# Kernel tuning notes

Measured on AMD Instinct MI355X. Metric: run time of the kernel, lower is better.

Reference implementation:

```python
import jax, jax.numpy as jnp
import numpy as np

DELTA = 1e-3  # inverse-distance kernel smoothing from NEC paper
NUM_NEIGHBOURS = 50


def setup_inputs() -> dict:
    key = jax.random.key(0)
    k1, k2, k3 = jax.random.split(key, 3)
    B, C, D = 1024, 500000, 64
    return {
        "keys": jax.random.normal(k1, (B, D), dtype=jnp.float32),
        "table_keys": jax.random.normal(k2, (C, D), dtype=jnp.float32),
        "table_values": jax.random.normal(k3, (C,), dtype=jnp.float32),
    }


def reference(keys, table_keys, table_values):
    # Brute-force kNN search: squared L2 distances [B, C]
    d2 = (
        jnp.sum(keys * keys, axis=1, keepdims=True)
        - 2.0 * (keys @ table_keys.T)
        + jnp.sum(table_keys * table_keys, axis=1)[None, :]
    )
    _, idx = jax.lax.top_k(-d2, NUM_NEIGHBOURS)  # [B, K] smallest distances

    neighbours = table_keys[idx]  # [B, K, D] gather
    # recompute exact squared distances against gathered neighbours
    sq = jnp.sum((keys[:, None, :] - neighbours) ** 2, axis=2)  # [B, K]
    w = 1.0 / (sq + DELTA)
    w = w / jnp.sum(w, axis=1, keepdims=True)
    v = table_values[idx]  # [B, K]
    return jnp.sum(w * v, axis=1)  # [B]
```

## Files before the change

### kernel.cpp

```cpp
#include <hip/hip_runtime.h>
#include <math.h>


#define DELTA_SMOOTH 1e-3f
#define K_NEIGH 50
#define MAXCAP 8192
#define NBINS 256
#define MARGIN_T 1.5f
#define MARGIN_Q 26
#define RPB 1024
#define QTILE 512
#define SDEPTH 6
#define LW 768
#define CVL 2048
#define S_SAMP 16384
#define T_SAMP 13
#define FSAMPLE 2048
#define FTARGET 6
#define FMARGIN 0.75f
#define FQB 4

typedef __attribute__((ext_vector_type(8))) short short8;
typedef __attribute__((ext_vector_type(4))) float f32x4;
typedef __attribute__((address_space(1))) const unsigned int g_u32;
typedef __attribute__((address_space(3))) unsigned int l_u32;

__device__ __forceinline__ unsigned f2bf(float f) {
  unsigned u = __float_as_uint(f);
  return ((u + 0x7fffu + ((u >> 16) & 1u)) >> 16) & 0xffffu;
}

__global__ __launch_bounds__(256) void convert_kernel(
    const float* __restrict__ tk, uint4* __restrict__ tkbf,
    float* __restrict__ tnh2, int C, int padded) {
  int t = blockIdx.x * 256 + threadIdx.x;
  int r = t >> 3;
  if (r >= padded) return;
  int c = t & 7;
  int rs = r < C ? r : C - 1;
  const float4* src = (const float4*)(tk + (size_t)rs * 64 + c * 8);
  float4 a = src[0], b = src[1];
  float sq = a.x * a.x + a.y * a.y + a.z * a.z + a.w * a.w
           + b.x * b.x + b.y * b.y + b.z * b.z + b.w * b.w;
  sq += __shfl_xor(sq, 1); sq += __shfl_xor(sq, 2); sq += __shfl_xor(sq, 4);
  if (c == 0) tnh2[r] = (r < C) ? sq * 0.5f : 3e38f;
  uint4 u;
  u.x = f2bf(a.x) | (f2bf(a.y) << 16);
  u.y = f2bf(a.z) | (f2bf(a.w) << 16);
  u.z = f2bf(b.x) | (f2bf(b.y) << 16);
  u.w = f2bf(b.z) | (f2bf(b.w) << 16);
  tkbf[(size_t)(r >> 6) * 512 + (r & 63) * 8 + (c ^ (r & 7))] = u;
}

__global__ __launch_bounds__(512, 4) void qthresh_mfma(
    const uint4* __restrict__ tkbf, const float* __restrict__ keys,
    const float* __restrict__ tnh2, unsigned short* __restrict__ dsamp) {
  __shared__ __align__(16) uint4 bstage[2][512];
  __shared__ float tnh_lds[128];
  int tid = threadIdx.x;
  int qt = blockIdx.x & 1;
  int chunk = blockIdx.x >> 1;
  int qbase = qt * QTILE;
  int rstart = chunk * 128;
  if (tid < 128) tnh_lds[tid] = tnh2[rstart + tid];
  int lane = tid & 63, wq = tid >> 6, l15 = lane & 15, quad = lane >> 4;
  short8 afrag[4][2];
  #pragma unroll
  for (int mt = 0; mt < 4; ++mt) {
    const float* kp = keys + (size_t)(qbase + wq * 64 + mt * 16 + l15) * 64 + quad * 8;
    #pragma unroll
    for (int s = 0; s < 2; ++s) {
      float4 x = *(const float4*)(kp + s * 32);
      float4 y = *(const float4*)(kp + s * 32 + 4);
      short8 a;
      a[0] = (short)f2bf(x.x); a[1] = (short)f2bf(x.y);
      a[2] = (short)f2bf(x.z); a[3] = (short)f2bf(x.w);
      a[4] = (short)f2bf(y.x); a[5] = (short)f2bf(y.y);
      a[6] = (short)f2bf(y.z); a[7] = (short)f2bf(y.w);
      afrag[mt][s] = a;
    }
  }
  const uint4* gbase = tkbf + (size_t)(rstart >> 6) * 512;
  __builtin_amdgcn_global_load_lds((g_u32*)(gbase + tid),
                                   (l_u32*)(&bstage[0][wq * 64]), 16, 0, 0);
  __syncthreads();
  f32x4 zero4 = {0.f, 0.f, 0.f, 0.f};
  for (int it = 0; it < 2; ++it) {
    if (it == 0)
      __builtin_amdgcn_global_load_lds((g_u32*)(gbase + 512 + tid),
                                       (l_u32*)(&bstage[1][wq * 64]), 16, 0, 0);
    const unsigned char* buf = (const unsigned char*)bstage[it & 1];
    #pragma unroll
    for (int half = 0; half < 2; ++half) {
      short8 b[2][2];
      #pragma unroll
      for (int tt = 0; tt < 2; ++tt) {
        int nloc = half * 32 + tt * 16 + l15;
        #pragma unroll
        for (int s = 0; s < 2; ++s) {
          int c = s * 4 + quad;
          unsigned addr = (unsigned)(nloc * 128 + ((c ^ (nloc & 7)) << 4));
          b[tt][s] = *(const short8*)(buf + addr);
        }
      }
      f32x4 acc[4][2];
      #pragma unroll
      for (int mt = 0; mt < 4; ++mt)
        #pragma unroll
        for (int tt = 0; tt < 2; ++tt) {
          f32x4 a0 = __builtin_amdgcn_mfma_f32_16x16x32_bf16(afrag[mt][0], b[tt][0], zero4, 0, 0, 0);
          acc[mt][tt] = __builtin_amdgcn_mfma_f32_16x16x32_bf16(afrag[mt][1], b[tt][1], a0, 0, 0, 0);
        }
      #pragma unroll
      for (int tt = 0; tt < 2; ++tt) {
        int rloc = it * 64 + half * 32 + tt * 16 + l15;
        float tnh = tnh_lds[rloc];
        int n = rstart + rloc;
        #pragma unroll
        for (int mt = 0; mt < 4; ++mt) {
          #pragma unroll
          for (int r = 0; r < 4; ++r) {
            int ql = wq * 64 + mt * 16 + quad * 4 + r;
            int u = (int)fmaf(tnh - acc[mt][tt][r], 512.f, 32768.f);
            u = u < 0 ? 0 : (u > 65535 ? 65535 : u);
            dsamp[(size_t)(qbase + ql) * S_SAMP + n] = (unsigned short)u;
          }
        }
      }
    }
    __syncthreads();
  }
}

__global__ __launch_bounds__(256) void qthresh_scan(
    const unsigned short* __restrict__ dsamp, float* __restrict__ thrh,
    int* __restrict__ cnt) {
  int q = blockIdx.x;
  __shared__ unsigned hist[512];
  int tid = threadIdx.x;
  hist[tid] = 0u; hist[tid + 256] = 0u;
  __syncthreads();
  const unsigned short* dp = dsamp + (size_t)q * S_SAMP;
  for (int i = tid; i < S_SAMP; i += 256) atomicAdd(&hist[dp[i] >> 7], 1u);
  __syncthreads();
  if (tid == 0) {
    unsigned cum = 0; int bstar = 511;
    for (int b = 0; b < 512; ++b) {
      cum += hist[b];
      if (cum >= (unsigned)T_SAMP) { bstar = b; break; }
    }
    float thr = (float)(bstar + 1) * 0.5f - 128.f + MARGIN_T;
    thrh[q] = 0.5f * thr;
    cnt[q] = 0;
  }
}

__global__ __launch_bounds__(512, 4) void filter_mfma_fast(
    const uint4* __restrict__ tkbf, const float* __restrict__ keys,
    const float* __restrict__ tnh2, const float* __restrict__ thrh,
    int* __restrict__ cnt, unsigned* __restrict__ candi, int C, int cap) {
  __shared__ __align__(16) uint4 bstage[4][512];
  __shared__ float tnh_lds[RPB];
  __shared__ float thr_lds[QTILE];
  __shared__ unsigned scnt[QTILE];
  __shared__ unsigned sbuf[QTILE * SDEPTH];

  int tid = threadIdx.x;
  int qt = blockIdx.x & 1;
  int chunk = blockIdx.x >> 1;
  int qbase = qt * QTILE;
  int rstart = chunk * RPB;

  tnh_lds[tid] = tnh2[rstart + tid];
  tnh_lds[tid + 512] = tnh2[rstart + tid + 512];
  thr_lds[tid] = thrh[qbase + tid];
  scnt[tid] = 0u;

  int lane = tid & 63, wq = tid >> 6, l15 = lane & 15, quad = lane >> 4;

  short8 afrag[4][2];
  #pragma unroll
  for (int mt = 0; mt < 4; ++mt) {
    const float* kp = keys + (size_t)(qbase + wq * 64 + mt * 16 + l15) * 64 + quad * 8;
    #pragma unroll
    for (int s = 0; s < 2; ++s) {
      float4 x = *(const float4*)(kp + s * 32);
      float4 y = *(const float4*)(kp + s * 32 + 4);
      short8 a;
      a[0] = (short)f2bf(x.x); a[1] = (short)f2bf(x.y);
      a[2] = (short)f2bf(x.z); a[3] = (short)f2bf(x.w);
      a[4] = (short)f2bf(y.x); a[5] = (short)f2bf(y.y);
      a[6] = (short)f2bf(y.z); a[7] = (short)f2bf(y.w);
      afrag[mt][s] = a;
    }
  }

  __syncthreads();

  float thrr[4][4];
  #pragma unroll
  for (int mt = 0; mt < 4; ++mt)
    #pragma unroll
    for (int r = 0; r < 4; ++r)
      thrr[mt][r] = thr_lds[wq * 64 + mt * 16 + quad * 4 + r];

  const uint4* gbase = tkbf + (size_t)(rstart >> 6) * 512;
  const int PHASES = RPB / 128;
  #pragma unroll
  for (int s = 0; s < 2; ++s)
    __builtin_amdgcn_global_load_lds((g_u32*)(gbase + (size_t)s * 512 + tid),
                                     (l_u32*)(&bstage[s][wq * 64]), 16, 0, 0);

  f32x4 zero4 = {0.f, 0.f, 0.f, 0.f};

  for (int ph = 0; ph < PHASES; ++ph) {
    __builtin_amdgcn_s_barrier();
    if (ph + 1 < PHASES) {
      #pragma unroll
      for (int s = 0; s < 2; ++s)
        __builtin_amdgcn_global_load_lds(
            (g_u32*)(gbase + ((size_t)(ph + 1) * 2 + s) * 512 + tid),
            (l_u32*)(&bstage[(((ph + 1) * 2 + s)) & 3][wq * 64]), 16, 0, 0);
      asm volatile("s_waitcnt vmcnt(2)" ::: "memory");
    } else {
      asm volatile("s_waitcnt vmcnt(0)" ::: "memory");
    }
    __builtin_amdgcn_sched_barrier(0);
    #pragma unroll
    for (int sl = 0; sl < 2; ++sl) {
      const unsigned char* buf = (const unsigned char*)bstage[(ph * 2 + sl) & 3];
      int itrow = ph * 128 + sl * 64;
      #pragma unroll
      for (int half = 0; half < 2; ++half) {
        short8 b[2][2];
        #pragma unroll
        for (int tt = 0; tt < 2; ++tt) {
          int nloc = half * 32 + tt * 16 + l15;
          #pragma unroll
          for (int s = 0; s < 2; ++s) {
            int c = s * 4 + quad;
            unsigned addr = (unsigned)(nloc * 128 + ((c ^ (nloc & 7)) << 4));
            b[tt][s] = *(const short8*)(buf + addr);
          }
        }
        f32x4 acc[4][2];
        #pragma unroll
        for (int mt = 0; mt < 4; ++mt)
          #pragma unroll
          for (int tt = 0; tt < 2; ++tt) {
            f32x4 a0 = __builtin_amdgcn_mfma_f32_16x16x32_bf16(afrag[mt][0], b[tt][0], zero4, 0, 0, 0);
            acc[mt][tt] = __builtin_amdgcn_mfma_f32_16x16x32_bf16(afrag[mt][1], b[tt][1], a0, 0, 0, 0);
          }
        #pragma unroll
        for (int tt = 0; tt < 2; ++tt) {
          int rloc = itrow + half * 32 + tt * 16 + l15;
          float tnh = tnh_lds[rloc];
          int n = rstart + rloc;
          #pragma unroll
          for (int mt = 0; mt < 4; ++mt) {
            #pragma unroll
            for (int r = 0; r < 4; ++r) {
              float t = tnh - acc[mt][tt][r];
              if (__builtin_expect(t < thrr[mt][r], 0)) {
                int ql = wq * 64 + mt * 16 + quad * 4 + r;
                int d2q = (int)fmaf(t, 32.f, 2048.f);
                d2q = d2q < 0 ? 0 : (d2q > 8191 ? 8191 : d2q);
                unsigned v = ((unsigned)d2q << 19) | (unsigned)n;
                unsigned p = atomicAdd(&scnt[ql], 1u);
                if (p < SDEPTH) {
                  sbuf[ql * SDEPTH + p] = v;
                } else {
                  int g = atomicAdd(&cnt[qbase + ql], 1);
                  if (g < cap) candi[(size_t)(qbase + ql) * cap + g] = v;
                }
              }
            }
          }
        }
      }
    }
  }
  __syncthreads();
  int m = (int)scnt[tid];
  if (m > SDEPTH) m = SDEPTH;
  if (m > 0) {
    int base = atomicAdd(&cnt[qbase + tid], m);
    for (int j = 0; j < m; ++j) {
      int g = base + j;
      if (g < cap) candi[(size_t)(qbase + tid) * cap + g] = sbuf[tid * SDEPTH + j];
    }
  }
}

__global__ __launch_bounds__(256) void qthresh_fb(
    const float* __restrict__ keys, const float* __restrict__ tk,
    float* __restrict__ thr, float* __restrict__ qnorm, int C) {
  int q0 = blockIdx.x * FQB;
  __shared__ __align__(16) float kq[FQB * 64];
  __shared__ unsigned hist[FQB][NBINS];
  __shared__ float qn4[FQB];
  int tid = threadIdx.x;
  for (int i = tid; i < FQB * 64; i += 256) kq[i] = keys[(size_t)q0 * 64 + i];
  for (int i = tid; i < FQB * NBINS; i += 256) (&hist[0][0])[i] = 0u;
  __syncthreads();
  if (tid < FQB) {
    float s = 0.f;
    for (int j = 0; j < 64; ++j) { float v = kq[tid * 64 + j]; s += v * v; }
    qn4[tid] = s;
  }
  __syncthreads();
  int kc = tid & 3;
  const float4* kq4 = (const float4*)kq;
  float4 kf[FQB][4];
  #pragma unroll
  for (int jq = 0; jq < FQB; ++jq)
    #pragma unroll
    for (int u = 0; u < 4; ++u) kf[jq][u] = kq4[jq * 16 + kc * 4 + u];
  int S = FSAMPLE < C ? FSAMPLE : C;
  for (int r = tid >> 2; r < S; r += 64) {
    const float4* trow = (const float4*)(tk + (size_t)r * 64 + kc * 16);
    float4 t0 = trow[0], t1 = trow[1], t2 = trow[2], t3 = trow[3];
    float tn = t0.x * t0.x + t0.y * t0.y + t0.z * t0.z + t0.w * t0.w
             + t1.x * t1.x + t1.y * t1.y + t1.z * t1.z + t1.w * t1.w
             + t2.x * t2.x + t2.y * t2.y + t2.z * t2.z + t2.w * t2.w
             + t3.x * t3.x + t3.y * t3.y + t3.z * t3.z + t3.w * t3.w;
    tn += __shfl_xor(tn, 1); tn += __shfl_xor(tn, 2);
    float dot[FQB];
    #pragma unroll
    for (int jq = 0; jq < FQB; ++jq) {
      float s = kf[jq][0].x * t0.x + kf[jq][0].y * t0.y + kf[jq][0].z * t0.z + kf[jq][0].w * t0.w
              + kf[jq][1].x * t1.x + kf[jq][1].y * t1.y + kf[jq][1].z * t1.z + kf[jq][1].w * t1.w
              + kf[jq][2].x * t2.x + kf[jq][2].y * t2.y + kf[jq][2].z * t2.z + kf[jq][2].w * t2.w
              + kf[jq][3].x * t3.x + kf[jq][3].y * t3.y + kf[jq][3].z * t3.z + kf[jq][3].w * t3.w;
      s += __shfl_xor(s, 1); s += __shfl_xor(s, 2);
      dot[jq] = s;
    }
    if (kc == 0) {
      #pragma unroll
      for (int jq = 0; jq < FQB; ++jq) {
        float d2 = qn4[jq] + tn - 2.f * dot[jq];
        int b = (int)d2;
        b = b < 0 ? 0 : (b > NBINS - 1 ? NBINS - 1 : b);
        atomicAdd(&hist[jq][b], 1u);
      }
    }
  }
  __syncthreads();
  if (tid < FQB) {
    unsigned cum = 0; int bstar = NBINS - 1;
    for (int b = 0; b < NBINS; ++b) {
      cum += hist[tid][b];
      if (cum >= (unsigned)FTARGET) { bstar = b; break; }
    }
    thr[q0 + tid] = (float)(bstar + 1) + FMARGIN - qn4[tid];
    qnorm[q0 + tid] = qn4[tid];
  }
}

__global__ __launch_bounds__(512, 4) void filter_fb(
    const float* __restrict__ keys, const float* __restrict__ tk,
    const float* __restrict__ thr, const float* __restrict__ qnorm,
    int* __restrict__ cnt, unsigned* __restrict__ candi, int C, int cap) {
  __shared__ float tnstage[64];
  __shared__ float thr_lds[QTILE];
  __shared__ float qn_lds[QTILE];
  __shared__ unsigned scnt[QTILE];
  __shared__ unsigned sbuf[QTILE * SDEPTH];
  __shared__ __align__(16) unsigned char bstage[64 * 128];
  int tid = threadIdx.x;
  int qt = blockIdx.x & 1;
  int chunk = blockIdx.x >> 1;
  int qbase = qt * QTILE;
  int rstart = chunk * RPB;
  thr_lds[tid] = thr[qbase + tid];
  qn_lds[tid] = qnorm[qbase + tid];
  scnt[tid] = 0u;
  int lane = tid & 63, wq = tid >> 6, l15 = lane & 15, quad = lane >> 4;
  short8 afrag[4][2];
  #pragma unroll
  for (int mt = 0; mt < 4; ++mt) {
    const float* kp = keys + (size_t)(qbase + wq * 64 + mt * 16 + l15) * 64 + quad * 8;
    #pragma unroll
    for (int s = 0; s < 2; ++s) {
      float4 x = *(const float4*)(kp + s * 32);
      float4 y = *(const float4*)(kp + s * 32 + 4);
      short8 a;
      a[0] = (short)f2bf(x.x); a[1] = (short)f2bf(x.y);
      a[2] = (short)f2bf(x.z); a[3] = (short)f2bf(x.w);
      a[4] = (short)f2bf(y.x); a[5] = (short)f2bf(y.y);
      a[6] = (short)f2bf(y.z); a[7] = (short)f2bf(y.w);
      afrag[mt][s] = a;
    }
  }
  __syncthreads();
  float hq[4];
  #pragma unroll
  for (int mt = 0; mt < 4; ++mt) {
    float h0 = thr_lds[wq * 64 + mt * 16 + quad * 4 + 0];
    float h1 = thr_lds[wq * 64 + mt * 16 + quad * 4 + 1];
    float h2 = thr_lds[wq * 64 + mt * 16 + quad * 4 + 2];
    float h3 = thr_lds[wq * 64 + mt * 16 + quad * 4 + 3];
    hq[mt] = fmaxf(fmaxf(h0, h1), fmaxf(h2, h3));
  }
  int srow = tid >> 3, scol = tid & 7;
  unsigned sbyte = (unsigned)(srow * 128 + ((scol ^ (srow & 7)) << 4));
  const int ITERS = RPB / 64;
  int r0 = rstart + srow; if (r0 > C - 1) r0 = C - 1;
  float4 pa = *(const float4*)(tk + (size_t)r0 * 64 + scol * 8);
  float4 pb = *(const float4*)(tk + (size_t)r0 * 64 + scol * 8 + 4);
  f32x4 zero4 = {0.f, 0.f, 0.f, 0.f};
  for (int it = 0; it < ITERS; ++it) {
    float part = pa.x * pa.x + pa.y * pa.y + pa.z * pa.z + pa.w * pa.w
               + pb.x * pb.x + pb.y * pb.y + pb.z * pb.z + pb.w * pb.w;
    part += __shfl_xor(part, 1); part += __shfl_xor(part, 2); part += __shfl_xor(part, 4);
    if ((tid & 7) == 0) tnstage[srow] = part;
    uint4 u;
    u.x = f2bf(pa.x) | (f2bf(pa.y) << 16);
    u.y = f2bf(pa.z) | (f2bf(pa.w) << 16);
    u.z = f2bf(pb.x) | (f2bf(pb.y) << 16);
    u.w = f2bf(pb.z) | (f2bf(pb.w) << 16);
    *(uint4*)(bstage + sbyte) = u;
    __syncthreads();
    if (it + 1 < ITERS) {
      int rn = rstart + (it + 1) * 64 + srow; if (rn > C - 1) rn = C - 1;
      pa = *(const float4*)(tk + (size_t)rn * 64 + scol * 8);
      pb = *(const float4*)(tk + (size_t)rn * 64 + scol * 8 + 4);
    }
    #pragma unroll
    for (int half = 0; half < 2; ++half) {
      short8 b[2][2];
      #pragma unroll
      for (int tt = 0; tt < 2; ++tt) {
        int nloc = half * 32 + tt * 16 + l15;
        #pragma unroll
        for (int s = 0; s < 2; ++s) {
          int c = s * 4 + quad;
          unsigned addr = (unsigned)(nloc * 128 + ((c ^ (nloc & 7)) << 4));
          b[tt][s] = *(const short8*)(bstage + addr);
        }
      }
      f32x4 acc[4][2];
      #pragma unroll
      for (int mt = 0; mt < 4; ++mt)
        #pragma unroll
        for (int tt = 0; tt < 2; ++tt) {
          f32x4 a0 = __builtin_amdgcn_mfma_f32_16x16x32_bf16(afrag[mt][0], b[tt][0], zero4, 0, 0, 0);
          acc[mt][tt] = __builtin_amdgcn_mfma_f32_16x16x32_bf16(afrag[mt][1], b[tt][1], a0, 0, 0, 0);
        }
      #pragma unroll
      for (int tt = 0; tt < 2; ++tt) {
        float tn = tnstage[half * 32 + tt * 16 + l15];
        int n = rstart + it * 64 + half * 32 + tt * 16 + l15;
        #pragma unroll
        for (int mt = 0; mt < 4; ++mt) {
          float d0 = fmaf(-2.f, acc[mt][tt][0], tn);
          float d1 = fmaf(-2.f, acc[mt][tt][1], tn);
          float d2 = fmaf(-2.f, acc[mt][tt][2], tn);
          float d3 = fmaf(-2.f, acc[mt][tt][3], tn);
          float mn4 = fminf(fminf(d0, d1), fminf(d2, d3));
          if (mn4 < hq[mt]) {
            float dd[4] = {d0, d1, d2, d3};
            #pragma unroll
            for (int r = 0; r < 4; ++r) {
              int ql = wq * 64 + mt * 16 + quad * 4 + r;
              if (dd[r] < thr_lds[ql] && n < C) {
                float d2f = dd[r] + qn_lds[ql];
                int d2q = (int)(d2f * 16.f);
                d2q = d2q < 0 ? 0 : (d2q > 8191 ? 8191 : d2q);
                unsigned v = ((unsigned)d2q << 19) | (unsigned)n;
                unsigned p = atomicAdd(&scnt[ql], 1u);
                if (p < SDEPTH) sbuf[ql * SDEPTH + p] = v;
                else {
                  int g = atomicAdd(&cnt[qbase + ql], 1);
                  if (g < cap) candi[(size_t)(qbase + ql) * cap + g] = v;
                }
              }
            }
          }
        }
      }
    }
    __syncthreads();
  }
  int m = (int)scnt[tid];
  if (m > SDEPTH) m = SDEPTH;
  if (m > 0) {
    int base = atomicAdd(&cnt[qbase + tid], m);
    for (int j = 0; j < m; ++j) {
      int g = base + j;
      if (g < cap) candi[(size_t)(qbase + tid) * cap + g] = sbuf[tid * SDEPTH + j];
    }
  }
}

__global__ __launch_bounds__(256) void select_kernel(
    const float* __restrict__ keys, const float* __restrict__ tk,
    const float* __restrict__ tv, const int* __restrict__ cnt,
    const unsigned* __restrict__ candi, float* __restrict__ out, int cap) {
  int q = blockIdx.x;
  __shared__ unsigned cvl[CVL];
  __shared__ unsigned hist[NBINS];
  __shared__ unsigned wsum[4];
  __shared__ unsigned minq_sh;
  __shared__ int b50_sh;
  __shared__ int lidx[LW];
  __shared__ unsigned ed2[LW];
  __shared__ int m_sh;
  __shared__ float redw[4], redwv[4];
  int tid = threadIdx.x;
  int lane = tid & 63;
  int wid = tid >> 6;
  int n = cnt[q];
  if (n > cap) n = cap;
  hist[tid] = 0u;
  if (tid == 0) { minq_sh = 0xffffffffu; b50_sh = NBINS - 1; m_sh = 0; }
  __syncthreads();
  const unsigned* cv = candi + (size_t)q * cap;
  unsigned mn = 0xffffffffu;
  for (int i = tid; i < n; i += 256) {
    unsigned v = cv[i];
    if (i < CVL) cvl[i] = v;
    unsigned d = v >> 19; if (d < mn) mn = d;
  }
  #pragma unroll
  for (int off = 1; off < 64; off <<= 1) { unsigned o = __shfl_xor(mn, off); if (o < mn) mn = o; }
  if (lane == 0) atomicMin(&minq_sh, mn);
  __syncthreads();
  unsigned base = minq_sh;
  for (int i = tid; i < n; i += 256) {
    unsigned v = (i < CVL) ? cvl[i] : cv[i];
    unsigned d = (v >> 19) - base;
    unsigned b = d >> 1; if (b > NBINS - 1) b = NBINS - 1;
    atomicAdd(&hist[b], 1u);
  }
  __syncthreads();
  unsigned h = hist[tid];
  unsigned p = h;
  #pragma unroll
  for (int off = 1; off < 64; off <<= 1) {
    unsigned v = __shfl_up(p, off);
    if (lane >= off) p += v;
  }
  if (lane == 63) wsum[wid] = p;
  __syncthreads();
  unsigned add = 0;
  for (int w2 = 0; w2 < wid; ++w2) add += wsum[w2];
  p += add;
  if (p >= (unsigned)K_NEIGH && p - h < (unsigned)K_NEIGH) b50_sh = tid;
  __syncthreads();
  unsigned Tq = base + (((unsigned)(b50_sh + 1)) << 1) + MARGIN_Q;
  for (int i = tid; i < n; i += 256) {
    unsigned v = (i < CVL) ? cvl[i] : cv[i];
    if ((v >> 19) <= Tq) {
      int p2 = atomicAdd(&m_sh, 1);
      if (p2 < LW) lidx[p2] = (int)(v & 0x7ffffu);
    }
  }
  __syncthreads();
  int m = m_sh; if (m > LW) m = LW;
  float kqv = keys[(size_t)q * 64 + lane];
  for (int i0 = wid * 4; i0 < m; i0 += 16) {
    int mm = m - i0; if (mm > 4) mm = 4;
    int idx[4]; float t[4];
    for (int u = 0; u < mm; ++u) idx[u] = lidx[i0 + u];
    for (int u = 0; u < mm; ++u) t[u] = tk[(size_t)idx[u] * 64 + lane];
    for (int u = 0; u < mm; ++u) {
      float d = t[u] - kqv;
      float s = d * d;
      #pragma unroll
      for (int off = 1; off < 64; off <<= 1) s += __shfl_xor(s, off);
      if (lane == 0) ed2[i0 + u] = __float_as_uint(s);
    }
  }
  __syncthreads();
  float accw = 0.f, accwv = 0.f;
  for (int i = tid; i < m; i += 256) {
    unsigned long long key = ((unsigned long long)ed2[i] << 19) | (unsigned)lidx[i];
    int rank = 0;
    for (int j = 0; j < m; ++j) {
      unsigned long long kj = ((unsigned long long)ed2[j] << 19) | (unsigned)lidx[j];
      rank += (kj < key) ? 1 : 0;
    }
    if (rank < K_NEIGH) {
      float d2 = __uint_as_float(ed2[i]);
      float w = 1.f / (d2 + DELTA_SMOOTH);
      accw += w;
      accwv += w * tv[lidx[i]];
    }
  }
  #pragma unroll
  for (int off = 1; off < 64; off <<= 1) {
    accw += __shfl_xor(accw, off);
    accwv += __shfl_xor(accwv, off);
  }
  if (lane == 0) { redw[wid] = accw; redwv[wid] = accwv; }
  __syncthreads();
  if (tid == 0) {
    float sw = redw[0] + redw[1] + redw[2] + redw[3];
    float swv = redwv[0] + redwv[1] + redwv[2] + redwv[3];
    out[q] = swv / sw;
  }
}

extern "C" void kernel_launch(void* const* d_in, const int* in_sizes, int n_in,
                              void* d_out, int out_size, void* d_ws, size_t ws_size,
                              hipStream_t stream) {
  const float* keys = (const float*)d_in[0];
  const float* tk   = (const float*)d_in[1];
  const float* tv   = (const float*)d_in[2];
  float* out = (float*)d_out;
  int B = in_sizes[0] / 64;
  int C = in_sizes[2];

  int nchunks = (C + RPB - 1) / RPB;
  int padded = nchunks * RPB;

  char* w = (char*)d_ws;
  float* thrh = (float*)w;  w += (size_t)B * 4;
  float* qnfb = (float*)w;  w += (size_t)B * 4;
  int*   cnt  = (int*)w;    w += (size_t)B * 4;
  size_t fixed = (size_t)(w - (char*)d_ws);

  size_t tk_bytes = (size_t)padded * 128 + (size_t)padded * 4;
  size_t dsamp_bytes = (size_t)S_SAMP * (size_t)B * 2;
  size_t region = ws_size > fixed + tk_bytes ? ws_size - fixed - tk_bytes : 0;
  bool fast = region >= dsamp_bytes && region >= 2048ull * (size_t)B * 4;

  if (fast) {
    uint4* tkbf = (uint4*)w;              w += (size_t)padded * 128;
    float* tnh2 = (float*)w;              w += (size_t)padded * 4;
    unsigned short* dsamp = (unsigned short*)w;
    unsigned* candi = (unsigned*)w;
    int cap = (int)(region / (4ull * (size_t)B));
    if (cap > MAXCAP) cap = MAXCAP;
    convert_kernel<<<(padded * 8 + 255) / 256, 256, 0, stream>>>(tk, tkbf, tnh2, C, padded);
    qthresh_mfma<<<256, 512, 0, stream>>>(tkbf, keys, tnh2, dsamp);
    qthresh_scan<<<B, 256, 0, stream>>>(dsamp, thrh, cnt);
    filter_mfma_fast<<<nchunks * 2, 512, 0, stream>>>(tkbf, keys, tnh2, thrh,
                                                      cnt, candi, C, cap);
    select_kernel<<<B, 256, 0, stream>>>(keys, tk, tv, cnt, candi, out, cap);
  } else {
    unsigned* candi = (unsigned*)w;
    int cap = (int)((ws_size - fixed) / (4ull * (size_t)B));
    if (cap > MAXCAP) cap = MAXCAP;
    if (cap < 1) cap = 1;
    hipMemsetAsync(cnt, 0, (size_t)B * 4, stream);
    qthresh_fb<<<B / FQB, 256, 0, stream>>>(keys, tk, thrh, qnfb, C);
    filter_fb<<<nchunks * 2, 512, 0, stream>>>(keys, tk, thrh, qnfb,
                                               cnt, candi, C, cap);
    select_kernel<<<B, 256, 0, stream>>>(keys, tk, tv, cnt, candi, out, cap);
  }
}
```

Baseline: 379.0 us.

## Cover all 1024 queries per filter block to halve table-tile loads

The filter kernel now runs 1024-thread blocks that each handle all 1024 queries against one 1024-row table chunk, instead of two 512-query blocks per chunk. Each bf16 table tile is loaded into LDS once rather than twice, cutting global traffic and the block count. The staging pipeline moves from per-128-row prefetch with partial waitcnt to double-buffered pairs with a full vmcnt(0)+barrier, and the per-query LDS spill depth drops from 6 to 4. The cost is higher LDS per block, lower occupancy, less load/compute overlap, and more global atomic overflow.

New measurement: 953.5 us. 2.52x slower.

```diff
diff --git a/kernel.cpp b/kernel.cpp
--- a/kernel.cpp
+++ b/kernel.cpp
@@ -9,6 +9,8 @@
 #define MARGIN_T 1.5f
 #define MARGIN_Q 26
 #define RPB 1024
+#define QB 1024
+#define SDF 4
 #define QTILE 512
 #define SDEPTH 6
 #define LW 768
@@ -60,7 +62,7 @@
   int tid = threadIdx.x;
   int qt = blockIdx.x & 1;
   int chunk = blockIdx.x >> 1;
-  int qbase = qt * QTILE;
+  int qbase = qt * 512;
   int rstart = chunk * 128;
   if (tid < 128) tnh_lds[tid] = tnh2[rstart + tid];
   int lane = tid & 63, wq = tid >> 6, l15 = lane & 15, quad = lane >> 4;
@@ -155,25 +157,21 @@
   }
 }
 
-__global__ __launch_bounds__(512, 4) void filter_mfma_fast(
+__global__ __launch_bounds__(1024, 8) void filter_mfma_fast(
     const uint4* __restrict__ tkbf, const float* __restrict__ keys,
     const float* __restrict__ tnh2, const float* __restrict__ thrh,
     int* __restrict__ cnt, unsigned* __restrict__ candi, int C, int cap) {
   __shared__ __align__(16) uint4 bstage[4][512];
   __shared__ float tnh_lds[RPB];
-  __shared__ float thr_lds[QTILE];
-  __shared__ unsigned scnt[QTILE];
-  __shared__ unsigned sbuf[QTILE * SDEPTH];
+  __shared__ float thr_lds[QB];
+  __shared__ unsigned scnt[QB];
+  __shared__ unsigned sbuf[QB * SDF];
 
   int tid = threadIdx.x;
-  int qt = blockIdx.x & 1;
-  int chunk = blockIdx.x >> 1;
-  int qbase = qt * QTILE;
-  int rstart = chunk * RPB;
+  int rstart = blockIdx.x * RPB;
 
   tnh_lds[tid] = tnh2[rstart + tid];
-  tnh_lds[tid + 512] = tnh2[rstart + tid + 512];
-  thr_lds[tid] = thrh[qbase + tid];
+  thr_lds[tid] = thrh[tid];
   scnt[tid] = 0u;
 
   int lane = tid & 63, wq = tid >> 6, l15 = lane & 15, quad = lane >> 4;
@@ -181,7 +179,7 @@
   short8 afrag[4][2];
   #pragma unroll
   for (int mt = 0; mt < 4; ++mt) {
-    const float* kp = keys + (size_t)(qbase + wq * 64 + mt * 16 + l15) * 64 + quad * 8;
+    const float* kp = keys + (size_t)(wq * 64 + mt * 16 + l15) * 64 + quad * 8;
     #pragma unroll
     for (int s = 0; s < 2; ++s) {
       float4 x = *(const float4*)(kp + s * 32);
@@ -205,31 +203,24 @@
       thrr[mt][r] = thr_lds[wq * 64 + mt * 16 + quad * 4 + r];
 
   const uint4* gbase = tkbf + (size_t)(rstart >> 6) * 512;
-  const int PHASES = RPB / 128;
-  #pragma unroll
-  for (int s = 0; s < 2; ++s)
-    __builtin_amdgcn_global_load_lds((g_u32*)(gbase + (size_t)s * 512 + tid),
-                                     (l_u32*)(&bstage[s][wq * 64]), 16, 0, 0);
+  const int PAIRS = RPB / 128;
+  __builtin_amdgcn_global_load_lds((g_u32*)(gbase + tid),
+                                   (l_u32*)((uint4*)&bstage[0][0] + wq * 64), 16, 0, 0);
 
   f32x4 zero4 = {0.f, 0.f, 0.f, 0.f};
 
-  for (int ph = 0; ph < PHASES; ++ph) {
-    __builtin_amdgcn_s_barrier();
-    if (ph + 1 < PHASES) {
-      #pragma unroll
-      for (int s = 0; s < 2; ++s)
-        __builtin_amdgcn_global_load_lds(
-            (g_u32*)(gbase + ((size_t)(ph + 1) * 2 + s) * 512 + tid),
-            (l_u32*)(&bstage[(((ph + 1) * 2 + s)) & 3][wq * 64]), 16, 0, 0);
-      asm volatile("s_waitcnt vmcnt(2)" ::: "memory");
-    } else {
-      asm volatile("s_waitcnt vmcnt(0)" ::: "memory");
-    }
+  for (int p = 0; p < PAIRS; ++p) {
+    asm volatile("s_waitcnt vmcnt(0)\n\ts_barrier" ::: "memory");
     __builtin_amdgcn_sched_barrier(0);
+    if (p + 1 < PAIRS) {
+      __builtin_amdgcn_global_load_lds(
+          (g_u32*)(gbase + (size_t)(p + 1) * 1024 + tid),
+          (l_u32*)((uint4*)&bstage[((p + 1) & 1) * 2][0] + wq * 64), 16, 0, 0);
+    }
     #pragma unroll
     for (int sl = 0; sl < 2; ++sl) {
-      const unsigned char* buf = (const unsigned char*)bstage[(ph * 2 + sl) & 3];
-      int itrow = ph * 128 + sl * 64;
+      const unsigned char* buf = (const unsigned char*)&bstage[(p & 1) * 2 + sl][0];
+      int itrow = p * 128 + sl * 64;
       #pragma unroll
       for (int half = 0; half < 2; ++half) {
         short8 b[2][2];
@@ -266,12 +257,12 @@
                 int d2q = (int)fmaf(t, 32.f, 2048.f);
                 d2q = d2q < 0 ? 0 : (d2q > 8191 ? 8191 : d2q);
                 unsigned v = ((unsigned)d2q << 19) | (unsigned)n;
-                unsigned p = atomicAdd(&scnt[ql], 1u);
-                if (p < SDEPTH) {
-                  sbuf[ql * SDEPTH + p] = v;
+                unsigned pp = atomicAdd(&scnt[ql], 1u);
+                if (pp < SDF) {
+                  sbuf[ql * SDF + pp] = v;
                 } else {
-                  int g = atomicAdd(&cnt[qbase + ql], 1);
-                  if (g < cap) candi[(size_t)(qbase + ql) * cap + g] = v;
+                  int g = atomicAdd(&cnt[ql], 1);
+                  if (g < cap) candi[(size_t)ql * cap + g] = v;
                 }
               }
             }
@@ -282,12 +273,12 @@
   }
   __syncthreads();
   int m = (int)scnt[tid];
-  if (m > SDEPTH) m = SDEPTH;
+  if (m > SDF) m = SDF;
   if (m > 0) {
-    int base = atomicAdd(&cnt[qbase + tid], m);
+    int base = atomicAdd(&cnt[tid], m);
     for (int j = 0; j < m; ++j) {
       int g = base + j;
-      if (g < cap) candi[(size_t)(qbase + tid) * cap + g] = sbuf[tid * SDEPTH + j];
+      if (g < cap) candi[(size_t)tid * cap + g] = sbuf[tid * SDF + j];
     }
   }
 }
@@ -636,8 +627,8 @@
     convert_kernel<<<(padded * 8 + 255) / 256, 256, 0, stream>>>(tk, tkbf, tnh2, C, padded);
     qthresh_mfma<<<256, 512, 0, stream>>>(tkbf, keys, tnh2, dsamp);
     qthresh_scan<<<B, 256, 0, stream>>>(dsamp, thrh, cnt);
-    filter_mfma_fast<<<nchunks * 2, 512, 0, stream>>>(tkbf, keys, tnh2, thrh,
-                                                      cnt, candi, C, cap);
+    filter_mfma_fast<<<nchunks, 1024, 0, stream>>>(tkbf, keys, tnh2, thrh,
+                                                   cnt, candi, C, cap);
     select_kernel<<<B, 256, 0, stream>>>(keys, tk, tv, cnt, candi, out, cap);
   } else {
     unsigned* candi = (unsigned*)w;
```

## Halve threshold sample, fold norm into MFMA accumulator, simplify filter pipeline

Applied to the files above, without the earlier changes.

Cuts the threshold-estimation sample from 16384 to 8192 rows (with a lower target rank) so the qthresh kernels do half the work. The filter kernel now seeds the MFMA accumulator with the negated half-norm, which removes a subtraction per output element, and compares against a negated threshold. Its prefetch loop changes to a wait-all-then-barrier pattern. The smaller sample may give a looser threshold and more candidates. Full waits could also expose load latency that the old partial wait hid.

After: 388.5 us. +2.5%, slower.

```diff
diff --git a/kernel.cpp b/kernel.cpp
--- a/kernel.cpp
+++ b/kernel.cpp
@@ -13,8 +13,8 @@
 #define SDEPTH 6
 #define LW 768
 #define CVL 2048
-#define S_SAMP 16384
-#define T_SAMP 13
+#define S_SAMP 8192
+#define T_SAMP 8
 #define FSAMPLE 2048
 #define FTARGET 6
 #define FMARGIN 0.75f
@@ -60,7 +60,7 @@
   int tid = threadIdx.x;
   int qt = blockIdx.x & 1;
   int chunk = blockIdx.x >> 1;
-  int qbase = qt * QTILE;
+  int qbase = qt * 512;
   int rstart = chunk * 128;
   if (tid < 128) tnh_lds[tid] = tnh2[rstart + tid];
   int lane = tid & 63, wq = tid >> 6, l15 = lane & 15, quad = lane >> 4;
@@ -197,41 +197,42 @@
 
   __syncthreads();
 
-  float thrr[4][4];
+  float negthr[4][4];
   #pragma unroll
   for (int mt = 0; mt < 4; ++mt)
     #pragma unroll
     for (int r = 0; r < 4; ++r)
-      thrr[mt][r] = thr_lds[wq * 64 + mt * 16 + quad * 4 + r];
+      negthr[mt][r] = -thr_lds[wq * 64 + mt * 16 + quad * 4 + r];
 
   const uint4* gbase = tkbf + (size_t)(rstart >> 6) * 512;
-  const int PHASES = RPB / 128;
+  const int PAIRS = RPB / 128;
   #pragma unroll
   for (int s = 0; s < 2; ++s)
     __builtin_amdgcn_global_load_lds((g_u32*)(gbase + (size_t)s * 512 + tid),
-                                     (l_u32*)(&bstage[s][wq * 64]), 16, 0, 0);
-
-  f32x4 zero4 = {0.f, 0.f, 0.f, 0.f};
-
-  for (int ph = 0; ph < PHASES; ++ph) {
-    __builtin_amdgcn_s_barrier();
-    if (ph + 1 < PHASES) {
-      #pragma unroll
-      for (int s = 0; s < 2; ++s)
+                                     (l_u32*)((uint4*)&bstage[s][0] + wq * 64), 16, 0, 0);
+
+  for (int p = 0; p < PAIRS; ++p) {
+    asm volatile("s_waitcnt vmcnt(0)\n\ts_barrier" ::: "memory");
+    __builtin_amdgcn_sched_barrier(0);
+    if (p + 1 < PAIRS) {
+      #pragma unroll
+      for (int s = 0; s < 2; ++s) {
+        int j = (p + 1) * 2 + s;
         __builtin_amdgcn_global_load_lds(
-            (g_u32*)(gbase + ((size_t)(ph + 1) * 2 + s) * 512 + tid),
-            (l_u32*)(&bstage[(((ph + 1) * 2 + s)) & 3][wq * 64]), 16, 0, 0);
-      asm volatile("s_waitcnt vmcnt(2)" ::: "memory");
-    } else {
-      asm volatile("s_waitcnt vmcnt(0)" ::: "memory");
-    }
-    __builtin_amdgcn_sched_barrier(0);
+            (g_u32*)(gbase + (size_t)j * 512 + tid),
+            (l_u32*)((uint4*)&bstage[j & 3][0] + wq * 64), 16, 0, 0);
+      }
+    }
     #pragma unroll
     for (int sl = 0; sl < 2; ++sl) {
-      const unsigned char* buf = (const unsigned char*)bstage[(ph * 2 + sl) & 3];
-      int itrow = ph * 128 + sl * 64;
+      const unsigned char* buf = (const unsigned char*)&bstage[(p * 2 + sl) & 3][0];
+      int itrow = p * 128 + sl * 64;
       #pragma unroll
       for (int half = 0; half < 2; ++half) {
+        float tnh0 = tnh_lds[itrow + half * 32 + l15];
+        float tnh1 = tnh_lds[itrow + half * 32 + 16 + l15];
+        f32x4 c0 = {-tnh0, -tnh0, -tnh0, -tnh0};
+        f32x4 c1 = {-tnh1, -tnh1, -tnh1, -tnh1};
         short8 b[2][2];
         #pragma unroll
         for (int tt = 0; tt < 2; ++tt) {
@@ -248,27 +249,27 @@
         for (int mt = 0; mt < 4; ++mt)
           #pragma unroll
           for (int tt = 0; tt < 2; ++tt) {
-            f32x4 a0 = __builtin_amdgcn_mfma_f32_16x16x32_bf16(afrag[mt][0], b[tt][0], zero4, 0, 0, 0);
-            acc[mt][tt] = __builtin_amdgcn_mfma_f32_16x16x32_bf16(afrag[mt][1], b[tt][1], a0, 0, 0, 0);
+            f32x4 a0 = __builtin_amdgcn_mfma_f32_16x16x32_bf16(
+                afrag[mt][0], b[tt][0], tt ? c1 : c0, 0, 0, 0);
+            acc[mt][tt] = __builtin_amdgcn_mfma_f32_16x16x32_bf16(
+                afrag[mt][1], b[tt][1], a0, 0, 0, 0);
           }
         #pragma unroll
         for (int tt = 0; tt < 2; ++tt) {
-          int rloc = itrow + half * 32 + tt * 16 + l15;
-          float tnh = tnh_lds[rloc];
-          int n = rstart + rloc;
+          int n = rstart + itrow + half * 32 + tt * 16 + l15;
           #pragma unroll
           for (int mt = 0; mt < 4; ++mt) {
             #pragma unroll
             for (int r = 0; r < 4; ++r) {
-              float t = tnh - acc[mt][tt][r];
-              if (__builtin_expect(t < thrr[mt][r], 0)) {
+              float a = acc[mt][tt][r];
+              if (__builtin_expect(a > negthr[mt][r], 0)) {
                 int ql = wq * 64 + mt * 16 + quad * 4 + r;
-                int d2q = (int)fmaf(t, 32.f, 2048.f);
+                int d2q = (int)fmaf(-a, 32.f, 2048.f);
                 d2q = d2q < 0 ? 0 : (d2q > 8191 ? 8191 : d2q);
                 unsigned v = ((unsigned)d2q << 19) | (unsigned)n;
-                unsigned p = atomicAdd(&scnt[ql], 1u);
-                if (p < SDEPTH) {
-                  sbuf[ql * SDEPTH + p] = v;
+                unsigned pp = atomicAdd(&scnt[ql], 1u);
+                if (pp < SDEPTH) {
+                  sbuf[ql * SDEPTH + pp] = v;
                 } else {
                   int g = atomicAdd(&cnt[qbase + ql], 1);
                   if (g < cap) candi[(size_t)(qbase + ql) * cap + g] = v;
@@ -634,7 +635,7 @@
     int cap = (int)(region / (4ull * (size_t)B));
     if (cap > MAXCAP) cap = MAXCAP;
     convert_kernel<<<(padded * 8 + 255) / 256, 256, 0, stream>>>(tk, tkbf, tnh2, C, padded);
-    qthresh_mfma<<<256, 512, 0, stream>>>(tkbf, keys, tnh2, dsamp);
+    qthresh_mfma<<<(S_SAMP / 128) * 2, 512, 0, stream>>>(tkbf, keys, tnh2, dsamp);
     qthresh_scan<<<B, 256, 0, stream>>>(dsamp, thrh, cnt);
     filter_mfma_fast<<<nchunks * 2, 512, 0, stream>>>(tkbf, keys, tnh2, thrh,
                                                       cnt, candi, C, cap);
```
